# Optimization experiments

Hardware: AMD Instinct MI355X
Metric: run time of the kernel (lower is better)

Reference implementation:

```python
import jax, jax.numpy as jnp
import numpy as np
from jax import lax

P_LEN, Q_LEN, B = 400, 60, 128
P_IN, Q_IN, H = 512, 512, 256
D = P_IN + Q_IN  # gate / GRU input size


def setup_inputs() -> dict:
    key = jax.random.key(0)
    ks = jax.random.split(key, 10)
    s = 0.05  # small init scale to keep tanh/sigmoid in sane range
    return {
        "q_input": jax.random.normal(ks[0], (Q_LEN, B, Q_IN), jnp.float32),
        "p_input": jax.random.normal(ks[1], (P_LEN, B, P_IN), jnp.float32),
        "q_mask": jnp.zeros((Q_LEN, B), dtype=bool),
        "Wq": jax.random.normal(ks[2], (2, Q_IN, H), jnp.float32) * s,
        "Wp": jax.random.normal(ks[3], (2, P_IN, H), jnp.float32) * s,
        "Ws": jax.random.normal(ks[4], (2, H, H), jnp.float32) * s,
        "v": jax.random.normal(ks[5], (2, H, 1), jnp.float32) * s,
        "gate_W": jax.random.normal(ks[6], (2, D, D), jnp.float32) * s,
        "gate_b": jnp.zeros((2, D), jnp.float32),
        "gru_Wih": jax.random.normal(ks[7], (2, 3 * H, D), jnp.float32) * s,
        "gru_Whh": jax.random.normal(ks[8], (2, 3 * H, H), jnp.float32) * s,
        "gru_bih": jnp.zeros((2, 3 * H), jnp.float32),
        "gru_bhh": jnp.zeros((2, 3 * H), jnp.float32),
    }


def _run_direction(q_input, p_input, q_mask, Wq, Wp, Ws, v,
                   gate_W, gate_b, gru_Wih, gru_Whh, gru_bih, gru_bhh,
                   reverse):
    # q_input: [Q, B, q_in], p_input: [P, B, p_in], q_mask: [Q, B] bool
    hid = Ws.shape[1]
    q_temp = jnp.einsum('qbe,eh->qbh', q_input, Wq)  # precomputed once, [Q,B,H]
    p_temp = jnp.einsum('pbe,eh->pbh', p_input, Wp)  # [P,B,H]
    mask = q_mask[:, :, None]                        # [Q,B,1]

    def step(state, xs):
        p_x, p_t = xs  # [B,p_in], [B,H]
        state_temp = state @ Ws                                   # [B,H]
        logits = jnp.tanh(q_temp + p_t[None] + state_temp[None]) @ v  # [Q,B,1]
        logits = jnp.where(mask, -jnp.inf, logits)
        weights = jax.nn.softmax(logits, axis=0)                  # over q_len
        att = jnp.sum(weights * q_input, axis=0)                  # [B,q_in]
        x = jnp.concatenate([p_x, att], axis=-1)                  # [B,D]
        x = x * jax.nn.sigmoid(x @ gate_W.T + gate_b)             # Gate
        # torch GRUCell math
        gi = x @ gru_Wih.T + gru_bih
        gh = state @ gru_Whh.T + gru_bhh
        i_r, i_z, i_n = jnp.split(gi, 3, axis=-1)
        h_r, h_z, h_n = jnp.split(gh, 3, axis=-1)
        r = jax.nn.sigmoid(i_r + h_r)
        z = jax.nn.sigmoid(i_z + h_z)
        n = jnp.tanh(i_n + r * h_n)
        new_state = (1.0 - z) * n + z * state
        return new_state, new_state

    init = jnp.zeros((p_input.shape[1], hid), p_input.dtype)
    _, out = lax.scan(step, init, (p_input, p_temp), reverse=reverse)
    return out  # [P,B,H], already in original time order (scan reverse handles it)


def reference(q_input, p_input, q_mask, Wq, Wp, Ws, v, gate_W, gate_b,
              gru_Wih, gru_Whh, gru_bih, gru_bhh):
    out_fw = _run_direction(q_input, p_input, q_mask, Wq[0], Wp[0], Ws[0], v[0],
                            gate_W[0], gate_b[0], gru_Wih[0], gru_Whh[0],
                            gru_bih[0], gru_bhh[0], reverse=False)
    out_bw = _run_direction(q_input, p_input, q_mask, Wq[1], Wp[1], Ws[1], v[1],
                            gate_W[1], gate_b[1], gru_Wih[1], gru_Whh[1],
                            gru_bih[1], gru_bhh[1], reverse=True)
    return jnp.concatenate([out_fw, out_bw], axis=-1)  # [P,B,2H]
```

## Files before the change

### kernel.cpp

```cpp
#include <hip/hip_runtime.h>

#define PL 400
#define QL 60
#define BB 128
#define EE 512
#define HH 256
#define DD 1024
#define G3 768
#define NBLK 256
#define NTHR 512
#define LDK 72

typedef __attribute__((ext_vector_type(8))) short bfrag;
typedef __attribute__((ext_vector_type(4))) float facc;

__device__ __forceinline__ unsigned short f2bf(float x) {
  unsigned u = __float_as_uint(x);
  return (unsigned short)((u + 0x7fffu + ((u >> 16) & 1u)) >> 16);
}
__device__ __forceinline__ float bf2f(unsigned short h) {
  return __uint_as_float(((unsigned)h) << 16);
}
__device__ __forceinline__ void split_bf(float x, unsigned short& hi, unsigned short& lo) {
  hi = f2bf(x);
  lo = f2bf(x - bf2f(hi));
}
__device__ __forceinline__ unsigned packf(float x) {
  unsigned short hi, lo;
  split_bf(x, hi, lo);
  return ((unsigned)hi << 16) | lo;
}
__device__ __forceinline__ float unpk(unsigned p) {
  return bf2f((unsigned short)(p >> 16)) + bf2f((unsigned short)(p & 0xffffu));
}
__device__ __forceinline__ float sigm(float x) {
  return __builtin_amdgcn_rcpf(1.f + __expf(-x));
}
__device__ __forceinline__ float ftanh(float x) {
  float xc = fminf(fmaxf(x, -10.f), 10.f);
  float t = __expf(2.f * xc);
  return (t - 1.f) * __builtin_amdgcn_rcpf(t + 1.f);
}

__device__ __forceinline__ float ald(const float* p) {
  return __hip_atomic_load((float*)p, __ATOMIC_RELAXED, __HIP_MEMORY_SCOPE_AGENT);
}
__device__ __forceinline__ void ast(float* p, float v) {
  __hip_atomic_store(p, v, __ATOMIC_RELAXED, __HIP_MEMORY_SCOPE_AGENT);
}
__device__ __forceinline__ unsigned aldu(const unsigned* p) {
  return __hip_atomic_load((unsigned*)p, __ATOMIC_RELAXED, __HIP_MEMORY_SCOPE_AGENT);
}
__device__ __forceinline__ void astu(unsigned* p, unsigned v) {
  __hip_atomic_store(p, v, __ATOMIC_RELAXED, __HIP_MEMORY_SCOPE_AGENT);
}
__device__ __forceinline__ void pollge(unsigned* f, unsigned tgt) {
  unsigned sp = 0;
  while (aldu(f) < tgt) {
    __builtin_amdgcn_s_sleep(1);
    if (++sp > (1u << 26)) break;
  }
}

constexpr size_t SZ_QT  = (size_t)2 * QL * BB * HH;
constexpr size_t SZ_PT  = (size_t)2 * PL * BB * HH;
constexpr size_t SZ_GIP = (size_t)2 * 4 * BB * G3;
constexpr size_t SZ_GHP = (size_t)2 * BB * G3;
constexpr size_t SZ_WST = (size_t)2 * HH * HH;
constexpr size_t OFF_QT  = 0;
constexpr size_t OFF_PT  = OFF_QT + SZ_QT;
constexpr size_t OFF_GIP = OFF_PT + SZ_PT;
constexpr size_t OFF_GHP = OFF_GIP + SZ_GIP;
constexpr size_t OFF_WST = OFF_GHP + SZ_GHP;
constexpr size_t F32_TOT = OFF_WST + SZ_WST;
constexpr size_t UOFF_ATTP  = 0;
constexpr size_t UOFF_XPACK = UOFF_ATTP + (size_t)2 * 2 * BB * EE;
constexpr size_t UOFF_HPACK = UOFF_XPACK + (size_t)2 * 2 * BB * DD;
constexpr size_t U_TOT      = UOFF_HPACK + (size_t)2 * BB * HH;
constexpr size_t HSZ_WQT = (size_t)2 * HH * EE;
constexpr size_t HSZ_GW  = (size_t)2 * DD * DD;
constexpr size_t HSZ_WIH = (size_t)2 * G3 * DD;
constexpr size_t HSZ_WHH = (size_t)2 * G3 * HH;
constexpr size_t HOFF_WQTH = 0;
constexpr size_t HOFF_WQTL = HOFF_WQTH + HSZ_WQT;
constexpr size_t HOFF_WPTH = HOFF_WQTL + HSZ_WQT;
constexpr size_t HOFF_WPTL = HOFF_WPTH + HSZ_WQT;
constexpr size_t HOFF_GWH  = HOFF_WPTL + HSZ_WQT;
constexpr size_t HOFF_GWL  = HOFF_GWH + HSZ_GW;
constexpr size_t HOFF_WIHH = HOFF_GWL + HSZ_GW;
constexpr size_t HOFF_WIHL = HOFF_WIHH + HSZ_WIH;
constexpr size_t HOFF_WHHH = HOFF_WIHL + HSZ_WIH;
constexpr size_t HOFF_WHHL = HOFF_WHHH + HSZ_WHH;
constexpr size_t H_TOT     = HOFF_WHHL + HSZ_WHH;

#define FA 0
#define FG 256
#define FI 320
#define FH 416
#define FC 440

__device__ __forceinline__ void gbar(unsigned* slots, unsigned gen) {
  asm volatile("" ::: "memory");
  __syncthreads();
  if (threadIdx.x == 0)
    __hip_atomic_store(&slots[blockIdx.x], gen, __ATOMIC_RELAXED, __HIP_MEMORY_SCOPE_AGENT);
  if (threadIdx.x < NBLK) pollge(&slots[threadIdx.x], gen);
  __syncthreads();
  asm volatile("" ::: "memory");
}

template <int NT, bool BSPLIT, int AMODE, int NCH>
__device__ void gemm_core(facc* acc, unsigned short* sAh, unsigned short* sAl,
                          const unsigned short* wh, const unsigned short* wl,
                          const float* a32, const unsigned* apk, int as,
                          int kbase, int wchbase) {
  const int tid = threadIdx.x;
  const int lane = tid & 63;
  const int w = tid >> 6;
  constexpr int FM = 2;
  constexpr int FN = (NT == 32) ? 1 : 2;
  const int wm = (w >> 1) << 5;
  const int wn = (NT == 64) ? ((w & 1) << 5) : ((w & 1) << 4);
  const int lr = lane & 15;
  const int lk = (lane >> 4) << 3;

  unsigned pva[16], pvb[16];
#pragma unroll
  for (int ii = 0; ii < 16; ii++) {
    int r = ii * 8 + w;
    pva[ii] = (AMODE == 0) ? __float_as_uint(a32[(size_t)r * as + kbase + lane])
                           : aldu(&apk[(size_t)r * as + kbase + lane]);
  }
#pragma unroll
  for (int ch = 0; ch < NCH; ++ch) {
    unsigned* cur = (ch & 1) ? pvb : pva;
    unsigned* nxt = (ch & 1) ? pva : pvb;
    if (ch + 1 < NCH) {
      const int kk1 = kbase + (ch + 1) * 64;
#pragma unroll
      for (int ii = 0; ii < 16; ii++) {
        int r = ii * 8 + w;
        nxt[ii] = (AMODE == 0) ? __float_as_uint(a32[(size_t)r * as + kk1 + lane])
                               : aldu(&apk[(size_t)r * as + kk1 + lane]);
      }
    }
#pragma unroll
    for (int ii = 0; ii < 16; ii++) {
      int r = ii * 8 + w;
      unsigned p = cur[ii];
      unsigned short uh, ul;
      if (AMODE == 0) split_bf(__uint_as_float(p), uh, ul);
      else { uh = (unsigned short)(p >> 16); ul = (unsigned short)(p & 0xffffu); }
      sAh[r * LDK + lane] = uh;
      sAl[r * LDK + lane] = ul;
    }
    asm volatile("s_waitcnt lgkmcnt(0)" ::: "memory");
    __builtin_amdgcn_s_barrier();
    __builtin_amdgcn_sched_barrier(0);
    const int wch = wchbase + ch;
#pragma unroll
    for (int k32 = 0; k32 < 64; k32 += 32) {
      bfrag ah[FM], al_[FM], bhf[FN], blf[FN];
#pragma unroll
      for (int f = 0; f < FM; f++) {
        const int ao = (wm + (f << 4) + lr) * LDK + k32 + lk;
        ah[f]  = *(const bfrag*)&sAh[ao];
        al_[f] = *(const bfrag*)&sAl[ao];
      }
#pragma unroll
      for (int f = 0; f < FN; f++) {
        const int bo = (wch * NT + wn + (f << 4) + lr) * LDK + k32 + lk;
        bhf[f] = *(const bfrag*)&wh[bo];
        if constexpr (BSPLIT) blf[f] = *(const bfrag*)&wl[bo];
      }
#pragma unroll
      for (int i = 0; i < FM; i++)
#pragma unroll
        for (int j = 0; j < FN; j++) {
          acc[i * FN + j] = __builtin_amdgcn_mfma_f32_16x16x32_bf16(al_[i], bhf[j], acc[i * FN + j], 0, 0, 0);
          if constexpr (BSPLIT)
            acc[i * FN + j] = __builtin_amdgcn_mfma_f32_16x16x32_bf16(ah[i], blf[j], acc[i * FN + j], 0, 0, 0);
          acc[i * FN + j] = __builtin_amdgcn_mfma_f32_16x16x32_bf16(ah[i], bhf[j], acc[i * FN + j], 0, 0, 0);
        }
    }
    __builtin_amdgcn_sched_barrier(0);
    __builtin_amdgcn_s_barrier();
    __builtin_amdgcn_sched_barrier(0);
  }
}

__device__ void gemm_pro(unsigned short* sAh, unsigned short* sAl, unsigned short* warea,
                         const float* a32,
                         const unsigned short* bh_g, const unsigned short* bl_g,
                         float* dst) {
  const int tid = threadIdx.x;
  const int lane = tid & 63;
  const int w = tid >> 6;
  const int wm = (w >> 2) << 6;
  const int wn = (w & 3) << 5;
  const int lr = lane & 15;
  const int lk = (lane >> 4) << 3;
  unsigned short* wh = warea;
  unsigned short* wl = warea + 128 * LDK;
  const facc fz = {0.f, 0.f, 0.f, 0.f};
  facc acc[4][2];
#pragma unroll
  for (int i = 0; i < 4; i++)
#pragma unroll
    for (int j = 0; j < 2; j++) acc[i][j] = fz;
  for (int ch = 0; ch < 8; ++ch) {
    const int kk0 = ch << 6;
    for (int i = tid; i < 8192; i += NTHR) {
      const int r = i >> 6, k = i & 63;
      unsigned short uh, ul;
      split_bf(a32[(size_t)r * EE + kk0 + k], uh, ul);
      sAh[r * LDK + k] = uh;
      sAl[r * LDK + k] = ul;
      wh[r * LDK + k] = bh_g[(size_t)r * EE + kk0 + k];
      wl[r * LDK + k] = bl_g[(size_t)r * EE + kk0 + k];
    }
    __syncthreads();
#pragma unroll
    for (int k32 = 0; k32 < 64; k32 += 32) {
      bfrag ah[4], al_[4], bhf[2], blf[2];
#pragma unroll
      for (int f = 0; f < 4; f++) {
        const int ao = (wm + (f << 4) + lr) * LDK + k32 + lk;
        ah[f]  = *(const bfrag*)&sAh[ao];
        al_[f] = *(const bfrag*)&sAl[ao];
      }
#pragma unroll
      for (int f = 0; f < 2; f++) {
        const int bo = (wn + (f << 4) + lr) * LDK + k32 + lk;
        bhf[f] = *(const bfrag*)&wh[bo];
        blf[f] = *(const bfrag*)&wl[bo];
      }
#pragma unroll
      for (int i = 0; i < 4; i++)
#pragma unroll
        for (int j = 0; j < 2; j++) {
          acc[i][j] = __builtin_amdgcn_mfma_f32_16x16x32_bf16(al_[i], bhf[j], acc[i][j], 0, 0, 0);
          acc[i][j] = __builtin_amdgcn_mfma_f32_16x16x32_bf16(ah[i], blf[j], acc[i][j], 0, 0, 0);
          acc[i][j] = __builtin_amdgcn_mfma_f32_16x16x32_bf16(ah[i], bhf[j], acc[i][j], 0, 0, 0);
        }
    }
    __syncthreads();
  }
  const int orow = (lane >> 4) << 2;
  const int ocol = lane & 15;
#pragma unroll
  for (int i = 0; i < 4; i++)
#pragma unroll
    for (int j = 0; j < 2; j++)
#pragma unroll
      for (int q = 0; q < 4; q++)
        dst[(size_t)(wm + (i << 4) + orow + q) * HH + (wn + (j << 4) + ocol)] = acc[i][j][q];
}

__global__ void __launch_bounds__(256) k_transpose_qp(
    const float* __restrict__ Wq, const float* __restrict__ Wp,
    unsigned short* __restrict__ wqth, unsigned short* __restrict__ wqtl,
    unsigned short* __restrict__ wpth, unsigned short* __restrict__ wptl) {
  __shared__ float tile[64 * 65];
  const int blk = blockIdx.x;
  const int mat = blk >> 6;
  const int rem = blk & 63;
  const int d = rem >> 5;
  const int rem2 = rem & 31;
  const int kt = rem2 >> 2;
  const int nt = rem2 & 3;
  const float* src = mat ? Wp : Wq;
  unsigned short* dh = mat ? wpth : wqth;
  unsigned short* dl = mat ? wptl : wqtl;
  const int tid = threadIdx.x;
  for (int i = tid; i < 4096; i += 256) {
    int kr = i >> 6, nc = i & 63;
    tile[kr * 65 + nc] = src[((size_t)d * EE + kt * 64 + kr) * HH + nt * 64 + nc];
  }
  __syncthreads();
  for (int i = tid; i < 4096; i += 256) {
    int n = i >> 6, k = i & 63;
    unsigned short hi, lo;
    split_bf(tile[k * 65 + n], hi, lo);
    size_t o = ((size_t)d * HH + nt * 64 + n) * EE + kt * 64 + k;
    dh[o] = hi; dl[o] = lo;
  }
}

__global__ void __launch_bounds__(256) k_split_w(
    const float* __restrict__ gw, const float* __restrict__ wih, const float* __restrict__ whh,
    unsigned short* __restrict__ gwh, unsigned short* __restrict__ gwl,
    unsigned short* __restrict__ wihh, unsigned short* __restrict__ wihl,
    unsigned short* __restrict__ whhh, unsigned short* __restrict__ whhl) {
  const size_t N1 = HSZ_GW, N2 = HSZ_WIH, N3 = HSZ_WHH;
  for (size_t i = (size_t)blockIdx.x * 256 + threadIdx.x; i < N1 + N2 + N3;
       i += (size_t)gridDim.x * 256) {
    float x; unsigned short *ph, *pl; size_t o;
    if (i < N1)           { o = i;           x = gw[o];  ph = gwh;  pl = gwl; }
    else if (i < N1 + N2) { o = i - N1;      x = wih[o]; ph = wihh; pl = wihl; }
    else                  { o = i - N1 - N2; x = whh[o]; ph = whhh; pl = whhl; }
    unsigned short hi, lo;
    split_bf(x, hi, lo);
    ph[o] = hi; pl[o] = lo;
  }
}

__global__ void __launch_bounds__(256) k_wst(const float* __restrict__ Ws,
                                             float* __restrict__ wst) {
  size_t i = (size_t)blockIdx.x * 256 + threadIdx.x;
  if (i >= SZ_WST) return;
  int d = (int)(i >> 16);
  int j = (int)((i >> 8) & 255);
  int k = (int)(i & 255);
  wst[i] = Ws[((size_t)d * HH + k) * HH + j];
}

__global__ void __launch_bounds__(NTHR, 1) pe_main(
    const float* __restrict__ qin, const float* __restrict__ pin,
    const unsigned char* __restrict__ qmask,
    const float* __restrict__ vvec, const float* __restrict__ gateb,
    const float* __restrict__ bih, const float* __restrict__ bhh,
    float* __restrict__ out,
    float* __restrict__ fws, unsigned* __restrict__ upck,
    unsigned short* __restrict__ hws, unsigned* __restrict__ bar) {
  __shared__ __align__(16) unsigned short smem[56320];
  unsigned short* sAh = smem;
  unsigned short* sAl = smem + 9216;
  unsigned short* warea = smem + 18432;
  float* fsm = (float*)smem;
  float* sv_perm   = (float*)(smem + 55296);
  float* sstv_perm = (float*)(smem + 55808);

  float* qt   = fws + OFF_QT;
  float* pt   = fws + OFF_PT;
  float* gip  = fws + OFF_GIP;
  float* ghp  = fws + OFF_GHP;
  float* wst  = fws + OFF_WST;
  unsigned* attp0 = upck + UOFF_ATTP;
  unsigned* xpck0 = upck + UOFF_XPACK;
  unsigned* hpack = upck + UOFF_HPACK;
  unsigned short* wqth = hws + HOFF_WQTH;
  unsigned short* wqtl = hws + HOFF_WQTL;
  unsigned short* wpth = hws + HOFF_WPTH;
  unsigned short* wptl = hws + HOFF_WPTL;
  unsigned short* gwh  = hws + HOFF_GWH;
  unsigned short* wihh = hws + HOFF_WIHH;
  unsigned short* wihl = hws + HOFF_WIHL;
  unsigned short* whhh = hws + HOFF_WHHH;
  unsigned short* whhl = hws + HOFF_WHHL;
  unsigned* flg = bar + 256;

  const int blk = blockIdx.x;
  const int tid = threadIdx.x;
  const int lane = tid & 63;
  const int w = tid >> 6;

  const bool isGate = (blk < 64);
  const bool isGi   = (blk >= 64 && blk < 160);
  const bool isGh   = (blk >= 160 && blk < 184);
  const int gd = blk >> 5, gct = blk & 31, coloff = gct * 32;
  const int gi_g = blk - 64, id_ = gi_g / 48, ir = gi_g % 48;
  const int int_ = ir >> 2, iks = ir & 3;
  const int gh_g = blk - 160, hd = gh_g / 12, hnt = gh_g % 12;

  for (int tt = blk; tt < 1840; tt += NBLK) {
    if (tt < 1600) {
      int d = tt / 800, rem = tt % 800, mt = rem >> 1, ntp = rem & 1;
      gemm_pro(sAh, sAl, warea, pin + (size_t)mt * BB * EE,
               wpth + ((size_t)d * HH + ntp * 128) * EE,
               wptl + ((size_t)d * HH + ntp * 128) * EE,
               pt + ((size_t)d * PL * BB + (size_t)mt * BB) * HH + ntp * 128);
    } else {
      int u2 = tt - 1600;
      int d = u2 / 120, rem = u2 % 120, mt = rem >> 1, ntp = rem & 1;
      gemm_pro(sAh, sAl, warea, qin + (size_t)mt * BB * EE,
               wqth + ((size_t)d * HH + ntp * 128) * EE,
               wqtl + ((size_t)d * HH + ntp * 128) * EE,
               qt + ((size_t)d * QL * BB + (size_t)mt * BB) * HH + ntp * 128);
    }
  }

  if (isGate) {
    const unsigned short* src = gwh + (size_t)(gd * DD + coloff) * DD;
    for (int i = tid; i < 32768; i += NTHR) {
      int ch = i >> 11, n = (i >> 6) & 31, k = i & 63;
      warea[(ch * 32 + n) * LDK + k] = src[(size_t)n * DD + ch * 64 + k];
    }
  } else if (isGi) {
    const unsigned short* sh = wihh + (size_t)(id_ * G3 + int_ * 64) * DD + iks * 256;
    const unsigned short* sl = wihl + (size_t)(id_ * G3 + int_ * 64) * DD + iks * 256;
    for (int i = tid; i < 16384; i += NTHR) {
      int ch = i >> 12, n = (i >> 6) & 63, k = i & 63;
      warea[(ch * 64 + n) * LDK + k]         = sh[(size_t)n * DD + ch * 64 + k];
      warea[18432 + (ch * 64 + n) * LDK + k] = sl[(size_t)n * DD + ch * 64 + k];
    }
  } else if (isGh) {
    const unsigned short* sh = whhh + (size_t)(hd * G3 + hnt * 64) * HH;
    const unsigned short* sl = whhl + (size_t)(hd * G3 + hnt * 64) * HH;
    for (int i = tid; i < 16384; i += NTHR) {
      int ch = i >> 12, n = (i >> 6) & 63, k = i & 63;
      warea[(ch * 64 + n) * LDK + k]         = sh[(size_t)n * HH + ch * 64 + k];
      warea[18432 + (ch * 64 + n) * LDK + k] = sl[(size_t)n * HH + ch * 64 + k];
    }
  }

  __builtin_amdgcn_fence(__ATOMIC_RELEASE, "agent");
  gbar(bar, 1);

  const int d_ab = blk >> 7, b_ab = blk & 127;
  if (tid < 256) {
    sv_perm[tid] = vvec[d_ab * HH + tid];
    sstv_perm[tid] = 0.f;
  }
  const bool qmv = (tid < 64 && lane < QL) ? (qmask[lane * BB + b_ab] != 0) : false;
  __syncthreads();

  facc pinacc[2];
  if (isGate) {
    const facc fz = {0.f, 0.f, 0.f, 0.f};
    pinacc[0] = fz; pinacc[1] = fz;
    const int t0 = gd ? (PL - 1) : 0;
    gemm_core<32, false, 0, 8>(pinacc, sAh, sAl, warea, nullptr,
                               pin + (size_t)t0 * BB * EE, nullptr, EE, 0, 0);
  }

  float hreg = 0.f;
  float* sm = fsm;
  float* slog = fsm + 512;
  float* swgt = fsm + 576;
  float* spart = fsm + 896;
  float* hrow = fsm + 1408;

  for (int s = 0; s < PL; ++s) {
    const int par = s & 1;
    unsigned* attp = attp0 + (size_t)par * 2 * BB * EE;
    unsigned* xpack = xpck0 + (size_t)par * 2 * BB * DD;
    const unsigned gen = (unsigned)(s + 1);

    {
      const int d = d_ab, b = b_ab;
      const int t = d ? (PL - 1 - s) : s;
      if (tid < 256) {
        float ptv = __builtin_nontemporal_load(&pt[(((size_t)d * PL + t) * BB + b) * HH + tid]);
        sm[tid] = sstv_perm[tid] + ptv;
      }
      __syncthreads();
      for (int q = w; q < QL; q += 8) {
        float a = 0.f;
#pragma unroll
        for (int jj = 0; jj < 4; jj++) {
          int j = lane + jj * 64;
          a += ftanh(qt[(((size_t)d * QL + q) * BB + b) * HH + j] + sm[j]) * sv_perm[j];
        }
        for (int off = 32; off; off >>= 1) a += __shfl_down(a, off, 64);
        if (lane == 0) slog[q] = a;
      }
      __syncthreads();
      if (tid < 64) {
        float x = -3.0e38f;
        if (lane < QL) {
          x = slog[lane];
          if (qmv) x = -3.0e38f;
        }
        float mx = x;
        for (int off = 32; off; off >>= 1) mx = fmaxf(mx, __shfl_xor(mx, off, 64));
        float e = (lane < QL) ? __expf(x - mx) : 0.f;
        float sum2 = e;
        for (int off = 32; off; off >>= 1) sum2 += __shfl_xor(sum2, off, 64);
        if (lane < QL) swgt[lane] = e * __builtin_amdgcn_rcpf(sum2);
      }
      __syncthreads();
      {
        const int c = tid;
        float a0 = 0.f, a1 = 0.f, a2 = 0.f, a3 = 0.f;
        const float* qb = qin + (size_t)b * EE + c;
        for (int q = 0; q < QL; q += 4) {
          a0 += swgt[q]     * qb[(size_t)q * BB * EE];
          a1 += swgt[q + 1] * qb[(size_t)(q + 1) * BB * EE];
          a2 += swgt[q + 2] * qb[(size_t)(q + 2) * BB * EE];
          a3 += swgt[q + 3] * qb[(size_t)(q + 3) * BB * EE];
        }
        astu(&attp[((size_t)d * BB + b) * EE + c], packf((a0 + a1) + (a2 + a3)));
      }
      __syncthreads();
      if (tid == 0) astu(&flg[FA + d_ab * 128 + b_ab], gen);
    }

    if (isGate) {
      if (tid < 128) pollge(&flg[FA + gd * 128 + tid], gen);
      __syncthreads();
      gemm_core<32, false, 1, 8>(pinacc, sAh, sAl, warea, nullptr,
                                 nullptr, attp + (size_t)gd * BB * EE, EE, 0, 8);
      {
        const int t = gd ? (PL - 1 - s) : s;
        const float* pin_t = pin + (size_t)t * BB * EE;
        const int wm2 = (w >> 1) << 5;
        const int wn2 = (w & 1) << 4;
        const int orow = (lane >> 4) << 2;
        const int ocol = lane & 15;
#pragma unroll
        for (int i = 0; i < 2; i++)
#pragma unroll
          for (int q = 0; q < 4; q++) {
            const int row = wm2 + (i << 4) + orow + q;
            const int gcol = coloff + wn2 + ocol;
            float uv = (gct < 16) ? pin_t[(size_t)row * EE + gcol]
                                  : unpk(aldu(&attp[((size_t)gd * BB + row) * EE + gcol - EE]));
            float x = uv * sigm(pinacc[i][q] + gateb[(size_t)gd * DD + gcol]);
            astu(&xpack[((size_t)gd * BB + row) * DD + gcol], packf(x));
          }
      }
      __syncthreads();
      if (tid == 0) astu(&flg[FG + gd * 32 + gct], gen);
      if (s + 1 < PL) {
        const facc fz = {0.f, 0.f, 0.f, 0.f};
        pinacc[0] = fz; pinacc[1] = fz;
        const int t2 = gd ? (PL - 2 - s) : (s + 1);
        gemm_core<32, false, 0, 8>(pinacc, sAh, sAl, warea, nullptr,
                                   pin + (size_t)t2 * BB * EE, nullptr, EE, 0, 0);
      }
    } else if (isGi) {
      if (tid < 8) pollge(&flg[FG + id_ * 32 + iks * 8 + tid], gen);
      __syncthreads();
      const facc fz = {0.f, 0.f, 0.f, 0.f};
      facc acc[4] = {fz, fz, fz, fz};
      gemm_core<64, true, 1, 4>(acc, sAh, sAl, warea, warea + 18432,
                                nullptr, xpack + (size_t)id_ * BB * DD, DD, iks * 256, 0);
      {
        const int wm2 = (w >> 1) << 5;
        const int wn2 = (w & 1) << 5;
        const int orow = (lane >> 4) << 2;
        const int ocol = lane & 15;
#pragma unroll
        for (int i = 0; i < 2; i++)
#pragma unroll
          for (int j = 0; j < 2; j++)
#pragma unroll
            for (int q = 0; q < 4; q++) {
              const int row = wm2 + (i << 4) + orow + q;
              const int col = int_ * 64 + wn2 + (j << 4) + ocol;
              ast(&gip[((size_t)(id_ * 4 + iks) * BB + row) * G3 + col], acc[i * 2 + j][q]);
            }
      }
      __syncthreads();
      if (tid == 0) astu(&flg[FI + id_ * 48 + ir], gen);
    } else if (isGh) {
      if (s > 0 && tid < 128) pollge(&flg[FC + hd * 128 + tid], (unsigned)s);
      __syncthreads();
      const facc fz = {0.f, 0.f, 0.f, 0.f};
      facc acc[4] = {fz, fz, fz, fz};
      gemm_core<64, true, 1, 4>(acc, sAh, sAl, warea, warea + 18432,
                                nullptr, hpack + (size_t)hd * BB * HH, HH, 0, 0);
      {
        const int wm2 = (w >> 1) << 5;
        const int wn2 = (w & 1) << 5;
        const int orow = (lane >> 4) << 2;
        const int ocol = lane & 15;
#pragma unroll
        for (int i = 0; i < 2; i++)
#pragma unroll
          for (int j = 0; j < 2; j++)
#pragma unroll
            for (int q = 0; q < 4; q++) {
              const int row = wm2 + (i << 4) + orow + q;
              const int col = hnt * 64 + wn2 + (j << 4) + ocol;
              ast(&ghp[((size_t)hd * BB + row) * G3 + col], acc[i * 2 + j][q]);
            }
      }
      __syncthreads();
      if (tid == 0) astu(&flg[FH + hd * 12 + hnt], gen);
    }

    {
      if (tid < 48) pollge(&flg[FI + d_ab * 48 + tid], gen);
      else if (tid < 60) pollge(&flg[FH + d_ab * 12 + (tid - 48)], gen);
      __syncthreads();
      const int d = d_ab, b = b_ab;
      const int j = tid & 255, half = tid >> 8;
      const int t = d ? (PL - 1 - s) : s;
      const size_t rb = (size_t)d * BB + b;
      float gi3[3], gh3[3];
#pragma unroll
      for (int c3 = 0; c3 < 3; c3++) {
        float acc2 = bih[(size_t)d * G3 + c3 * HH + j];
#pragma unroll
        for (int ks = 0; ks < 4; ks++)
          acc2 += ald(&gip[((size_t)(d * 4 + ks) * BB + b) * G3 + c3 * HH + j]);
        gi3[c3] = acc2;
        gh3[c3] = ald(&ghp[rb * G3 + c3 * HH + j]) + bhh[(size_t)d * G3 + c3 * HH + j];
      }
      float r = sigm(gi3[0] + gh3[0]);
      float z = sigm(gi3[1] + gh3[1]);
      float n = ftanh(gi3[2] + r * gh3[2]);
      float hn = (1.f - z) * n + z * hreg;
      hreg = hn;
      if (half == 0) {
        out[((size_t)t * BB + b) * 512 + d * HH + j] = hn;
        astu(&hpack[rb * HH + j], packf(hn));
        hrow[j] = hn;
      }
      __syncthreads();
      if (tid == 0) astu(&flg[FC + d_ab * 128 + b_ab], gen);
      float part = 0.f;
      const float* wr = wst + ((size_t)d * HH + j) * HH + (half << 7);
      const float* hr = hrow + (half << 7);
#pragma unroll
      for (int k = 0; k < 128; k += 4) {
        float4 w4 = *(const float4*)&wr[k];
        float4 h4 = *(const float4*)&hr[k];
        part += w4.x * h4.x + w4.y * h4.y + w4.z * h4.z + w4.w * h4.w;
      }
      spart[tid] = part;
      __syncthreads();
      if (tid < 256) sstv_perm[tid] = spart[tid] + spart[tid + 256];
      __syncthreads();
    }
  }
}

extern "C" void kernel_launch(void* const* d_in, const int* in_sizes, int n_in,
                              void* d_out, int out_size, void* d_ws, size_t ws_size,
                              hipStream_t stream) {
  const float* qin = (const float*)d_in[0];
  const float* pin = (const float*)d_in[1];
  const unsigned char* qmask = (const unsigned char*)d_in[2];
  const float* Wq  = (const float*)d_in[3];
  const float* Wp  = (const float*)d_in[4];
  const float* Ws  = (const float*)d_in[5];
  const float* v   = (const float*)d_in[6];
  const float* gw  = (const float*)d_in[7];
  const float* gb  = (const float*)d_in[8];
  const float* wih = (const float*)d_in[9];
  const float* whh = (const float*)d_in[10];
  const float* bih = (const float*)d_in[11];
  const float* bhh = (const float*)d_in[12];
  float* out = (float*)d_out;

  char* base = (char*)d_ws;
  float* fws = (float*)base;
  unsigned* upck = (unsigned*)(base + F32_TOT * sizeof(float));
  unsigned short* hws = (unsigned short*)(base + F32_TOT * sizeof(float) + U_TOT * sizeof(unsigned));
  unsigned* bar = (unsigned*)(base + F32_TOT * sizeof(float) + U_TOT * sizeof(unsigned) +
                              H_TOT * sizeof(unsigned short));
  size_t need = F32_TOT * sizeof(float) + U_TOT * sizeof(unsigned) +
                H_TOT * sizeof(unsigned short) + 8192;
  if (ws_size < need) return;

  hipMemsetAsync(upck + UOFF_HPACK, 0, (size_t)2 * BB * HH * sizeof(unsigned), stream);
  hipMemsetAsync(bar, 0, 4096, stream);

  k_transpose_qp<<<128, 256, 0, stream>>>(Wq, Wp,
      hws + HOFF_WQTH, hws + HOFF_WQTL, hws + HOFF_WPTH, hws + HOFF_WPTL);
  k_split_w<<<1024, 256, 0, stream>>>(gw, wih, whh,
      hws + HOFF_GWH, hws + HOFF_GWL, hws + HOFF_WIHH, hws + HOFF_WIHL,
      hws + HOFF_WHHH, hws + HOFF_WHHL);
  k_wst<<<(int)((SZ_WST + 255) / 256), 256, 0, stream>>>(Ws, fws + OFF_WST);
  pe_main<<<NBLK, NTHR, 0, stream>>>(qin, pin, qmask, v, gb, bih, bhh, out,
                                     fws, upck, hws, bar);
}
```

Measured before the change: 25.55 ms.

## Load GEMM A-operands directly into MFMA fragments and use bf16 q_input for attention

The shared-memory staging of the A operand in the step GEMMs is removed. Each wave now loads its 16-row fragment straight from global memory (packed hi/lo words or fp32 split on the fly), which drops two block barriers per K chunk. The wave tiling changes to 16 rows by NT columns per wave. The attention weighted sum reads a bf16 copy of q_input prepared in a preprocessing kernel, halving that traffic at the cost of precision. Output stores become nontemporal.

New measurement: 20.54 ms. 19.6% less time.

```diff
diff --git a/kernel.cpp b/kernel.cpp
--- a/kernel.cpp
+++ b/kernel.cpp
@@ -13,6 +13,7 @@
 
 typedef __attribute__((ext_vector_type(8))) short bfrag;
 typedef __attribute__((ext_vector_type(4))) float facc;
+typedef __attribute__((ext_vector_type(4))) unsigned uintx4;
 
 __device__ __forceinline__ unsigned short f2bf(float x) {
   unsigned u = __float_as_uint(x);
@@ -53,6 +54,9 @@
 }
 __device__ __forceinline__ void astu(unsigned* p, unsigned v) {
   __hip_atomic_store(p, v, __ATOMIC_RELAXED, __HIP_MEMORY_SCOPE_AGENT);
+}
+__device__ __forceinline__ unsigned long long aldull(const unsigned long long* p) {
+  return __hip_atomic_load((unsigned long long*)p, __ATOMIC_RELAXED, __HIP_MEMORY_SCOPE_AGENT);
 }
 __device__ __forceinline__ void pollge(unsigned* f, unsigned tgt) {
   unsigned sp = 0;
@@ -91,7 +95,8 @@
 constexpr size_t HOFF_WIHL = HOFF_WIHH + HSZ_WIH;
 constexpr size_t HOFF_WHHH = HOFF_WIHL + HSZ_WIH;
 constexpr size_t HOFF_WHHL = HOFF_WHHH + HSZ_WHH;
-constexpr size_t H_TOT     = HOFF_WHHL + HSZ_WHH;
+constexpr size_t HOFF_QIN16 = HOFF_WHHL + HSZ_WHH;
+constexpr size_t H_TOT      = HOFF_QIN16 + (size_t)QL * BB * EE;
 
 #define FA 0
 #define FG 256
@@ -109,83 +114,77 @@
   asm volatile("" ::: "memory");
 }
 
-template <int NT, bool BSPLIT, int AMODE, int NCH>
-__device__ void gemm_core(facc* acc, unsigned short* sAh, unsigned short* sAl,
-                          const unsigned short* wh, const unsigned short* wl,
-                          const float* a32, const unsigned* apk, int as,
-                          int kbase, int wchbase) {
+template <int NT, bool BSPLIT, int NCH, int ASRC>
+__device__ void gemm_direct(facc* acc,
+                            const unsigned short* wh, const unsigned short* wl,
+                            const unsigned* apk, const float* a32, int as,
+                            int kbase, int wchbase) {
   const int tid = threadIdx.x;
   const int lane = tid & 63;
   const int w = tid >> 6;
-  constexpr int FM = 2;
-  constexpr int FN = (NT == 32) ? 1 : 2;
-  const int wm = (w >> 1) << 5;
-  const int wn = (NT == 64) ? ((w & 1) << 5) : ((w & 1) << 4);
+  constexpr int FN = NT / 16;
   const int lr = lane & 15;
   const int lk = (lane >> 4) << 3;
-
-  unsigned pva[16], pvb[16];
-#pragma unroll
-  for (int ii = 0; ii < 16; ii++) {
-    int r = ii * 8 + w;
-    pva[ii] = (AMODE == 0) ? __float_as_uint(a32[(size_t)r * as + kbase + lane])
-                           : aldu(&apk[(size_t)r * as + kbase + lane]);
-  }
-#pragma unroll
+  const int row = (w << 4) + lr;
+
+#pragma unroll 2
   for (int ch = 0; ch < NCH; ++ch) {
-    unsigned* cur = (ch & 1) ? pvb : pva;
-    unsigned* nxt = (ch & 1) ? pva : pvb;
-    if (ch + 1 < NCH) {
-      const int kk1 = kbase + (ch + 1) * 64;
-#pragma unroll
-      for (int ii = 0; ii < 16; ii++) {
-        int r = ii * 8 + w;
-        nxt[ii] = (AMODE == 0) ? __float_as_uint(a32[(size_t)r * as + kk1 + lane])
-                               : aldu(&apk[(size_t)r * as + kk1 + lane]);
-      }
-    }
-#pragma unroll
-    for (int ii = 0; ii < 16; ii++) {
-      int r = ii * 8 + w;
-      unsigned p = cur[ii];
-      unsigned short uh, ul;
-      if (AMODE == 0) split_bf(__uint_as_float(p), uh, ul);
-      else { uh = (unsigned short)(p >> 16); ul = (unsigned short)(p & 0xffffu); }
-      sAh[r * LDK + lane] = uh;
-      sAl[r * LDK + lane] = ul;
-    }
-    asm volatile("s_waitcnt lgkmcnt(0)" ::: "memory");
-    __builtin_amdgcn_s_barrier();
-    __builtin_amdgcn_sched_barrier(0);
-    const int wch = wchbase + ch;
+    const int kk = kbase + (ch << 6);
 #pragma unroll
     for (int k32 = 0; k32 < 64; k32 += 32) {
-      bfrag ah[FM], al_[FM], bhf[FN], blf[FN];
-#pragma unroll
-      for (int f = 0; f < FM; f++) {
-        const int ao = (wm + (f << 4) + lr) * LDK + k32 + lk;
-        ah[f]  = *(const bfrag*)&sAh[ao];
-        al_[f] = *(const bfrag*)&sAl[ao];
-      }
+      const int ko = kk + k32 + lk;
+      bfrag ah, al_;
+      {
+        unsigned hu[4], lu[4];
+        if constexpr (ASRC == 0) {
+          const unsigned long long* src =
+              (const unsigned long long*)(apk + (size_t)row * as + ko);
+          unsigned long long d0 = aldull(src + 0);
+          unsigned long long d1 = aldull(src + 1);
+          unsigned long long d2 = aldull(src + 2);
+          unsigned long long d3 = aldull(src + 3);
+          unsigned p0 = (unsigned)d0, p1 = (unsigned)(d0 >> 32);
+          unsigned p2 = (unsigned)d1, p3 = (unsigned)(d1 >> 32);
+          unsigned p4 = (unsigned)d2, p5 = (unsigned)(d2 >> 32);
+          unsigned p6 = (unsigned)d3, p7 = (unsigned)(d3 >> 32);
+          hu[0] = (p0 >> 16) | (p1 & 0xffff0000u);  lu[0] = (p0 & 0xffffu) | (p1 << 16);
+          hu[1] = (p2 >> 16) | (p3 & 0xffff0000u);  lu[1] = (p2 & 0xffffu) | (p3 << 16);
+          hu[2] = (p4 >> 16) | (p5 & 0xffff0000u);  lu[2] = (p4 & 0xffffu) | (p5 << 16);
+          hu[3] = (p6 >> 16) | (p7 & 0xffff0000u);  lu[3] = (p6 & 0xffffu) | (p7 << 16);
+        } else {
+          const float* src = a32 + (size_t)row * as + ko;
+          float4 v0 = *(const float4*)src;
+          float4 v1 = *(const float4*)(src + 4);
+          unsigned short h0, l0, h1, l1;
+          split_bf(v0.x, h0, l0); split_bf(v0.y, h1, l1);
+          hu[0] = h0 | ((unsigned)h1 << 16); lu[0] = l0 | ((unsigned)l1 << 16);
+          split_bf(v0.z, h0, l0); split_bf(v0.w, h1, l1);
+          hu[1] = h0 | ((unsigned)h1 << 16); lu[1] = l0 | ((unsigned)l1 << 16);
+          split_bf(v1.x, h0, l0); split_bf(v1.y, h1, l1);
+          hu[2] = h0 | ((unsigned)h1 << 16); lu[2] = l0 | ((unsigned)l1 << 16);
+          split_bf(v1.z, h0, l0); split_bf(v1.w, h1, l1);
+          hu[3] = h0 | ((unsigned)h1 << 16); lu[3] = l0 | ((unsigned)l1 << 16);
+        }
+        uintx4 hv = {hu[0], hu[1], hu[2], hu[3]};
+        uintx4 lv = {lu[0], lu[1], lu[2], lu[3]};
+        ah  = __builtin_bit_cast(bfrag, hv);
+        al_ = __builtin_bit_cast(bfrag, lv);
+      }
+      bfrag bhf[FN], blf[FN];
 #pragma unroll
       for (int f = 0; f < FN; f++) {
-        const int bo = (wch * NT + wn + (f << 4) + lr) * LDK + k32 + lk;
+        const int bo = ((wchbase + ch) * NT + (f << 4) + lr) * LDK + k32 + lk;
         bhf[f] = *(const bfrag*)&wh[bo];
         if constexpr (BSPLIT) blf[f] = *(const bfrag*)&wl[bo];
       }
 #pragma unroll
-      for (int i = 0; i < FM; i++)
-#pragma unroll
-        for (int j = 0; j < FN; j++) {
-          acc[i * FN + j] = __builtin_amdgcn_mfma_f32_16x16x32_bf16(al_[i], bhf[j], acc[i * FN + j], 0, 0, 0);
-          if constexpr (BSPLIT)
-            acc[i * FN + j] = __builtin_amdgcn_mfma_f32_16x16x32_bf16(ah[i], blf[j], acc[i * FN + j], 0, 0, 0);
-          acc[i * FN + j] = __builtin_amdgcn_mfma_f32_16x16x32_bf16(ah[i], bhf[j], acc[i * FN + j], 0, 0, 0);
-        }
-    }
-    __builtin_amdgcn_sched_barrier(0);
-    __builtin_amdgcn_s_barrier();
-    __builtin_amdgcn_sched_barrier(0);
+      for (int j = 0; j < FN; j++) {
+        acc[j] = __builtin_amdgcn_mfma_f32_16x16x32_bf16(al_, bhf[j], acc[j], 0, 0, 0);
+        if constexpr (BSPLIT)
+          acc[j] = __builtin_amdgcn_mfma_f32_16x16x32_bf16(ah, blf[j], acc[j], 0, 0, 0);
+        acc[j] = __builtin_amdgcn_mfma_f32_16x16x32_bf16(ah, bhf[j], acc[j], 0, 0, 0);
+      }
+    }
   }
 }
 
@@ -305,14 +304,23 @@
   }
 }
 
-__global__ void __launch_bounds__(256) k_wst(const float* __restrict__ Ws,
-                                             float* __restrict__ wst) {
-  size_t i = (size_t)blockIdx.x * 256 + threadIdx.x;
-  if (i >= SZ_WST) return;
-  int d = (int)(i >> 16);
-  int j = (int)((i >> 8) & 255);
-  int k = (int)(i & 255);
-  wst[i] = Ws[((size_t)d * HH + k) * HH + j];
+__global__ void __launch_bounds__(256) k_wst_qin(const float* __restrict__ Ws,
+                                                 float* __restrict__ wst,
+                                                 const float* __restrict__ qin,
+                                                 unsigned short* __restrict__ qin16) {
+  const size_t NQ = (size_t)QL * BB * EE;
+  for (size_t i = (size_t)blockIdx.x * 256 + threadIdx.x; i < SZ_WST + NQ;
+       i += (size_t)gridDim.x * 256) {
+    if (i < SZ_WST) {
+      int d = (int)(i >> 16);
+      int j = (int)((i >> 8) & 255);
+      int k = (int)(i & 255);
+      wst[i] = Ws[((size_t)d * HH + k) * HH + j];
+    } else {
+      size_t o = i - SZ_WST;
+      qin16[o] = f2bf(qin[o]);
+    }
+  }
 }
 
 __global__ void __launch_bounds__(NTHR, 1) pe_main(
@@ -348,6 +356,7 @@
   unsigned short* wihl = hws + HOFF_WIHL;
   unsigned short* whhh = hws + HOFF_WHHH;
   unsigned short* whhl = hws + HOFF_WHHL;
+  const unsigned short* qin16 = hws + HOFF_QIN16;
   unsigned* flg = bar + 256;
 
   const int blk = blockIdx.x;
@@ -420,8 +429,8 @@
     const facc fz = {0.f, 0.f, 0.f, 0.f};
     pinacc[0] = fz; pinacc[1] = fz;
     const int t0 = gd ? (PL - 1) : 0;
-    gemm_core<32, false, 0, 8>(pinacc, sAh, sAl, warea, nullptr,
-                               pin + (size_t)t0 * BB * EE, nullptr, EE, 0, 0);
+    gemm_direct<32, false, 8, 1>(pinacc, warea, nullptr,
+                                 nullptr, pin + (size_t)t0 * BB * EE, EE, 0, 0);
   }
 
   float hreg = 0.f;
@@ -473,12 +482,12 @@
       {
         const int c = tid;
         float a0 = 0.f, a1 = 0.f, a2 = 0.f, a3 = 0.f;
-        const float* qb = qin + (size_t)b * EE + c;
+        const unsigned short* qb = qin16 + (size_t)b * EE + c;
         for (int q = 0; q < QL; q += 4) {
-          a0 += swgt[q]     * qb[(size_t)q * BB * EE];
-          a1 += swgt[q + 1] * qb[(size_t)(q + 1) * BB * EE];
-          a2 += swgt[q + 2] * qb[(size_t)(q + 2) * BB * EE];
-          a3 += swgt[q + 3] * qb[(size_t)(q + 3) * BB * EE];
+          a0 += swgt[q]     * bf2f(qb[(size_t)q * BB * EE]);
+          a1 += swgt[q + 1] * bf2f(qb[(size_t)(q + 1) * BB * EE]);
+          a2 += swgt[q + 2] * bf2f(qb[(size_t)(q + 2) * BB * EE]);
+          a3 += swgt[q + 3] * bf2f(qb[(size_t)(q + 3) * BB * EE]);
         }
         astu(&attp[((size_t)d * BB + b) * EE + c], packf((a0 + a1) + (a2 + a3)));
       }
@@ -486,24 +495,24 @@
       if (tid == 0) astu(&flg[FA + d_ab * 128 + b_ab], gen);
     }
 
+    const int orow = (lane >> 4) << 2;
+    const int ocol = lane & 15;
+    const int rbase = w << 4;
+
     if (isGate) {
       if (tid < 128) pollge(&flg[FA + gd * 128 + tid], gen);
       __syncthreads();
-      gemm_core<32, false, 1, 8>(pinacc, sAh, sAl, warea, nullptr,
-                                 nullptr, attp + (size_t)gd * BB * EE, EE, 0, 8);
+      gemm_direct<32, false, 8, 0>(pinacc, warea, nullptr,
+                                   attp + (size_t)gd * BB * EE, nullptr, EE, 0, 8);
       {
         const int t = gd ? (PL - 1 - s) : s;
         const float* pin_t = pin + (size_t)t * BB * EE;
-        const int wm2 = (w >> 1) << 5;
-        const int wn2 = (w & 1) << 4;
-        const int orow = (lane >> 4) << 2;
-        const int ocol = lane & 15;
 #pragma unroll
         for (int i = 0; i < 2; i++)
 #pragma unroll
           for (int q = 0; q < 4; q++) {
-            const int row = wm2 + (i << 4) + orow + q;
-            const int gcol = coloff + wn2 + ocol;
+            const int row = rbase + orow + q;
+            const int gcol = coloff + (i << 4) + ocol;
             float uv = (gct < 16) ? pin_t[(size_t)row * EE + gcol]
                                   : unpk(aldu(&attp[((size_t)gd * BB + row) * EE + gcol - EE]));
             float x = uv * sigm(pinacc[i][q] + gateb[(size_t)gd * DD + gcol]);
@@ -516,32 +525,24 @@
         const facc fz = {0.f, 0.f, 0.f, 0.f};
         pinacc[0] = fz; pinacc[1] = fz;
         const int t2 = gd ? (PL - 2 - s) : (s + 1);
-        gemm_core<32, false, 0, 8>(pinacc, sAh, sAl, warea, nullptr,
-                                   pin + (size_t)t2 * BB * EE, nullptr, EE, 0, 0);
+        gemm_direct<32, false, 8, 1>(pinacc, warea, nullptr,
+                                     nullptr, pin + (size_t)t2 * BB * EE, EE, 0, 0);
       }
     } else if (isGi) {
       if (tid < 8) pollge(&flg[FG + id_ * 32 + iks * 8 + tid], gen);
       __syncthreads();
       const facc fz = {0.f, 0.f, 0.f, 0.f};
       facc acc[4] = {fz, fz, fz, fz};
-      gemm_core<64, true, 1, 4>(acc, sAh, sAl, warea, warea + 18432,
-                                nullptr, xpack + (size_t)id_ * BB * DD, DD, iks * 256, 0);
-      {
-        const int wm2 = (w >> 1) << 5;
-        const int wn2 = (w & 1) << 5;
-        const int orow = (lane >> 4) << 2;
-        const int ocol = lane & 15;
-#pragma unroll
-        for (int i = 0; i < 2; i++)
-#pragma unroll
-          for (int j = 0; j < 2; j++)
-#pragma unroll
-            for (int q = 0; q < 4; q++) {
-              const int row = wm2 + (i << 4) + orow + q;
-              const int col = int_ * 64 + wn2 + (j << 4) + ocol;
-              ast(&gip[((size_t)(id_ * 4 + iks) * BB + row) * G3 + col], acc[i * 2 + j][q]);
-            }
-      }
+      gemm_direct<64, true, 4, 0>(acc, warea, warea + 18432,
+                                  xpack + (size_t)id_ * BB * DD, nullptr, DD, iks * 256, 0);
+#pragma unroll
+      for (int j = 0; j < 4; j++)
+#pragma unroll
+        for (int q = 0; q < 4; q++) {
+          const int row = rbase + orow + q;
+          const int col = int_ * 64 + (j << 4) + ocol;
+          ast(&gip[((size_t)(id_ * 4 + iks) * BB + row) * G3 + col], acc[j][q]);
+        }
       __syncthreads();
       if (tid == 0) astu(&flg[FI + id_ * 48 + ir], gen);
     } else if (isGh) {
@@ -549,24 +550,16 @@
       __syncthreads();
       const facc fz = {0.f, 0.f, 0.f, 0.f};
       facc acc[4] = {fz, fz, fz, fz};
-      gemm_core<64, true, 1, 4>(acc, sAh, sAl, warea, warea + 18432,
-                                nullptr, hpack + (size_t)hd * BB * HH, HH, 0, 0);
-      {
-        const int wm2 = (w >> 1) << 5;
-        const int wn2 = (w & 1) << 5;
-        const int orow = (lane >> 4) << 2;
-        const int ocol = lane & 15;
-#pragma unroll
-        for (int i = 0; i < 2; i++)
-#pragma unroll
-          for (int j = 0; j < 2; j++)
-#pragma unroll
-            for (int q = 0; q < 4; q++) {
-              const int row = wm2 + (i << 4) + orow + q;
-              const int col = hnt * 64 + wn2 + (j << 4) + ocol;
-              ast(&ghp[((size_t)hd * BB + row) * G3 + col], acc[i * 2 + j][q]);
-            }
-      }
+      gemm_direct<64, true, 4, 0>(acc, warea, warea + 18432,
+                                  hpack + (size_t)hd * BB * HH, nullptr, HH, 0, 0);
+#pragma unroll
+      for (int j = 0; j < 4; j++)
+#pragma unroll
+        for (int q = 0; q < 4; q++) {
+          const int row = rbase + orow + q;
+          const int col = hnt * 64 + (j << 4) + ocol;
+          ast(&ghp[((size_t)hd * BB + row) * G3 + col], acc[j][q]);
+        }
       __syncthreads();
       if (tid == 0) astu(&flg[FH + hd * 12 + hnt], gen);
     }
@@ -595,7 +588,7 @@
       float hn = (1.f - z) * n + z * hreg;
       hreg = hn;
       if (half == 0) {
-        out[((size_t)t * BB + b) * 512 + d * HH + j] = hn;
+        __builtin_nontemporal_store(hn, &out[((size_t)t * BB + b) * 512 + d * HH + j]);
         astu(&hpack[rb * HH + j], packf(hn));
         hrow[j] = hn;
       }
@@ -654,7 +647,8 @@
   k_split_w<<<1024, 256, 0, stream>>>(gw, wih, whh,
       hws + HOFF_GWH, hws + HOFF_GWL, hws + HOFF_WIHH, hws + HOFF_WIHL,
       hws + HOFF_WHHH, hws + HOFF_WHHL);
-  k_wst<<<(int)((SZ_WST + 255) / 256), 256, 0, stream>>>(Ws, fws + OFF_WST);
+  k_wst_qin<<<2048, 256, 0, stream>>>(Ws, fws + OFF_WST, qin,
+                                      hws + HOFF_QIN16);
   pe_main<<<NBLK, NTHR, 0, stream>>>(qin, pin, qmask, v, gb, bih, bhh, out,
                                      fws, upck, hws, bar);
 }
```
